# Performance work log

Hardware: AMD Instinct MI355X
Metric: run time of the kernel (lower is better)

## Reference

```python
import jax, jax.numpy as jnp
from jax import lax
import numpy as np

# ---- static config (matches init_kwargs) ----
B, H, W = 8, 32, 32
L = H * W                      # 1024 tokens
D_MODEL = 384
MAMBA_DIM = 192                # d_model * d_mamba_ratio
LOCAL_DIM = 192
D_INNER = 384                  # expand_m * MAMBA_DIM
D_STATE = 16
D_CONV = 4
DT_RANK = 12                   # ceil(MAMBA_DIM / 16)
NDIR = 4                       # h, h_flip, v, v_flip
RED = 48                       # int(D_INNER * 0.125), BiAttn reduce dim
INNER_C = 192                  # LOCAL_DIM * expand_c
K_C = 8                        # local block depthwise kernel size


def setup_inputs() -> dict:
    key = jax.random.key(0)
    ks = jax.random.split(key, 16)
    s = 0.02
    return {
        "x": jax.random.normal(ks[0], (B, L, D_MODEL), jnp.float32),
        "in_proj_w": jax.random.normal(ks[1], (2 * D_INNER, MAMBA_DIM)) * s,
        "A_log": jnp.broadcast_to(jnp.log(jnp.arange(1, D_STATE + 1, dtype=jnp.float32)), (NDIR, D_INNER, D_STATE)) + 0.0,
        "conv_w": jax.random.normal(ks[2], (NDIR, D_INNER, D_CONV)) * 0.2,
        "conv_b": jax.random.normal(ks[3], (NDIR, D_INNER)) * 0.02,
        "xproj_w": jax.random.normal(ks[4], (NDIR, DT_RANK + 2 * D_STATE, D_INNER)) * s,
        "dtproj_w": jax.random.normal(ks[5], (NDIR, D_INNER, DT_RANK)) * (DT_RANK ** -0.5),
        "dtproj_b": jax.random.normal(ks[6], (NDIR, D_INNER)) * 0.5 - 4.0,
        "Dp": jnp.ones((NDIR, D_INNER)),
        "out_proj_w": jax.random.normal(ks[7], (MAMBA_DIM, D_INNER)) * s,
        "attn_ln_g": jnp.ones((D_INNER,)),
        "attn_ln_b": jnp.zeros((D_INNER,)),
        "attn_gr_w": jax.random.normal(ks[8], (RED, D_INNER)) * s,
        "attn_gr_b": jnp.zeros((RED,)),
        "attn_cs_w": jax.random.normal(ks[9], (D_INNER, RED)) * s,
        "attn_cs_b": jnp.zeros((D_INNER,)),
        "pw1_w": jax.random.normal(ks[10], (2 * INNER_C, LOCAL_DIM)) * s,
        "pw1_b": jnp.zeros((2 * INNER_C,)),
        "dw_w": jax.random.normal(ks[11], (INNER_C, K_C)) * 0.2,
        "dw_b": jnp.zeros((INNER_C,)),
        "bn_g": jnp.ones((INNER_C,)),
        "bn_b": jnp.zeros((INNER_C,)),
        "pw2_w": jax.random.normal(ks[12], (LOCAL_DIM, INNER_C)) * s,
        "pw2_b": jnp.zeros((LOCAL_DIM,)),
    }


def _forward(x, in_proj_w, A_log, conv_w, conv_b, xproj_w, dtproj_w, dtproj_b, Dp,
             out_proj_w, attn_ln_g, attn_ln_b, attn_gr_w, attn_gr_b, attn_cs_w, attn_cs_b,
             pw1_w, pw1_b, dw_w, dw_b, bn_g, bn_b, pw2_w, pw2_b):
    mamba_in = x[:, :, :MAMBA_DIM]
    local_in = x[:, :, MAMBA_DIM:]

    # ---------- MultiMamba branch ----------
    xz = jnp.swapaxes(mamba_in @ in_proj_w.T, 1, 2)   # (B, 2*D_INNER, L)

    def to_dir(t, i):
        # reorder channel-last-token axis per scan direction
        if i == 0:
            return t
        if i == 1:
            return jnp.flip(t, -1)
        tv = t.reshape(B, -1, H, W).swapaxes(-1, -2).reshape(B, -1, L)  # column-major scan
        return tv if i == 2 else jnp.flip(tv, -1)

    def from_dir(t, i):
        if i == 0:
            return t
        if i == 1:
            return jnp.flip(t, -1)
        if i == 3:
            t = jnp.flip(t, -1)
        return t.reshape(B, -1, W, H).swapaxes(-1, -2).reshape(B, -1, L)

    def ssm_dir(xzd, i):
        # mamba_inner_fn_no_out_proj: causal dwconv -> silu -> x_proj -> selective scan -> gate
        xp, z = jnp.split(xzd, 2, axis=1)            # (B, D_INNER, L) each
        xpad = jnp.pad(xp, ((0, 0), (0, 0), (D_CONV - 1, 0)))
        u = lax.conv_general_dilated(xpad, conv_w[i][:, None, :], (1,), 'VALID',
                                     dimension_numbers=('NCH', 'OIH', 'NCH'),
                                     feature_group_count=D_INNER)
        u = jax.nn.silu(u + conv_b[i][None, :, None])
        dbl = jnp.einsum('bdl,rd->brl', u, xproj_w[i])
        dt = dbl[:, :DT_RANK]
        Bm = dbl[:, DT_RANK:DT_RANK + D_STATE]
        Cm = dbl[:, DT_RANK + D_STATE:]
        delta = jax.nn.softplus(jnp.einsum('brl,dr->bdl', dt, dtproj_w[i]) + dtproj_b[i][None, :, None])
        A = -jnp.exp(A_log[i])                        # (D_INNER, D_STATE)

        def step(h, inps):
            d_t, B_t, C_t, u_t = inps                 # (B,d),(B,n),(B,n),(B,d)
            h = jnp.exp(d_t[:, :, None] * A) * h + (d_t * u_t)[:, :, None] * B_t[:, None, :]
            return h, jnp.einsum('bdn,bn->bd', h, C_t)

        h0 = jnp.zeros((B, D_INNER, D_STATE), x.dtype)
        _, ys = lax.scan(step, h0, (delta.transpose(2, 0, 1), Bm.transpose(2, 0, 1),
                                    Cm.transpose(2, 0, 1), u.transpose(2, 0, 1)))
        y = ys.transpose(1, 2, 0) + u * Dp[i][:, None]  # (B, D_INNER, L)
        return y * jax.nn.silu(z)

    def biattn(t):                                     # (B, L, D_INNER)
        mu = t.mean(-1, keepdims=True)
        var = ((t - mu) ** 2).mean(-1, keepdims=True)
        tn = (t - mu) / jnp.sqrt(var + 1e-5) * attn_ln_g + attn_ln_b
        g = tn.mean(1, keepdims=True)                  # global pool (B,1,D_INNER)
        g = jax.nn.gelu(g @ attn_gr_w.T + attn_gr_b, approximate=False)
        c = jax.nn.sigmoid(g @ attn_cs_w.T + attn_cs_b)
        return t * c

    acc = jnp.zeros((B, L, D_INNER), x.dtype)
    for i in range(NDIR):                              # fixed small set of directions
        out_i = from_dir(ssm_dir(to_dir(xz, i), i), i)
        acc = acc + biattn(jnp.swapaxes(out_i, 1, 2))
    mamba_out = acc @ out_proj_w.T                     # (B, L, MAMBA_DIM)

    # ---------- Local conv branch ----------
    hch = jnp.einsum('blc,oc->bol', local_in, pw1_w) + pw1_b[None, :, None]
    a, gte = jnp.split(hch, 2, axis=1)
    hch = a * jax.nn.sigmoid(gte)                      # GLU, (B, INNER_C, L)
    pad_l = K_C // 2
    pad_r = K_C // 2 - (K_C + 1) % 2                   # calc_same_padding(8) -> (4, 3)
    hpad = jnp.pad(hch, ((0, 0), (0, 0), (pad_l, pad_r)))
    hch = lax.conv_general_dilated(hpad, dw_w[:, None, :], (1,), 'VALID',
                                   dimension_numbers=('NCH', 'OIH', 'NCH'),
                                   feature_group_count=INNER_C) + dw_b[None, :, None]
    mu = hch.mean((0, 2))                              # BatchNorm1d (training-mode batch stats)
    var = hch.var((0, 2))
    hch = (hch - mu[None, :, None]) / jnp.sqrt(var + 1e-5)[None, :, None] * bn_g[None, :, None] + bn_b[None, :, None]
    hch = hch * jax.nn.sigmoid(hch)                    # Swish
    local_out = jnp.einsum('bcl,oc->blo', hch, pw2_w) + pw2_b

    return jnp.concatenate([mamba_out, local_out], axis=-1)


def reference(x, in_proj_w, A_log, conv_w, conv_b, xproj_w, dtproj_w, dtproj_b, Dp,
              out_proj_w, attn_ln_g, attn_ln_b, attn_gr_w, attn_gr_b, attn_cs_w, attn_cs_b,
              pw1_w, pw1_b, dw_w, dw_b, bn_g, bn_b, pw2_w, pw2_b):
    return _forward(x, in_proj_w, A_log, conv_w, conv_b, xproj_w, dtproj_w, dtproj_b, Dp,
                    out_proj_w, attn_ln_g, attn_ln_b, attn_gr_w, attn_gr_b, attn_cs_w, attn_cs_b,
                    pw1_w, pw1_b, dw_w, dw_b, bn_g, bn_b, pw2_w, pw2_b)
```

## Files before the change

kernel.cpp:

```cpp
#include <hip/hip_runtime.h>
#include <stdint.h>


#define DEV __device__ __forceinline__

typedef __attribute__((ext_vector_type(8))) short short8;
typedef __attribute__((ext_vector_type(4))) short short4v;
typedef __attribute__((ext_vector_type(4))) float f32x4;

DEV float bf(ushort v) { union { uint32_t u; float f; } c; c.u = ((uint32_t)v) << 16; return c.f; }
DEV ushort fbf(float f) {
  union { float f; uint32_t u; } c; c.f = f;
  uint32_t u = c.u;
  return (ushort)((u + 0x7FFFu + ((u >> 16) & 1u)) >> 16);
}

#if __has_builtin(__builtin_amdgcn_exp2f)
DEV float fexp2(float x) { return __builtin_amdgcn_exp2f(x); }
#else
DEV float fexp2(float x) { return __expf(x * 0.6931471805599453f); }
#endif

template<int CTRL>
DEV float rradd(float x) {
  return x + __int_as_float(__builtin_amdgcn_update_dpp(
      0, __float_as_int(x), CTRL, 0xF, 0xF, true));
}

DEV int pmap(int i, int j) {
  if (i == 0) return j;
  if (i == 1) return 1023 - j;
  if (i == 2) return ((j & 31) << 5) | (j >> 5);
  int k = 1023 - j; return ((k & 31) << 5) | (k >> 5);
}

DEV void cvt4(const float* __restrict__ s, ushort* __restrict__ d, int blk, int tid) {
  const int idx = (blk * 256 + tid) * 4;
  float4 v = *(const float4*)(s + idx);
  d[idx] = fbf(v.x); d[idx + 1] = fbf(v.y); d[idx + 2] = fbf(v.z); d[idx + 3] = fbf(v.w);
}

__global__ __launch_bounds__(256) void prep_all(
    const float* __restrict__ x, ushort* __restrict__ xb,
    const float* __restrict__ ipw, ushort* __restrict__ ipwb,
    const float* __restrict__ opw, ushort* __restrict__ opwb,
    const float* __restrict__ pw1w, ushort* __restrict__ pw1wb,
    const float* __restrict__ pw2w, ushort* __restrict__ pw2wb,
    const float* __restrict__ xw, ushort* __restrict__ xwp)
{
  const int bx = blockIdx.x, tid = threadIdx.x;
  if (bx < 3072)      cvt4(x, xb, bx, tid);
  else if (bx < 3216) cvt4(ipw, ipwb, bx - 3072, tid);
  else if (bx < 3288) cvt4(opw, opwb, bx - 3216, tid);
  else if (bx < 3360) cvt4(pw1w, pw1wb, bx - 3288, tid);
  else if (bx < 3396) cvt4(pw2w, pw2wb, bx - 3360, tid);
  else {
    const int row = bx - 3396;
    const int i = row >> 6, nn = row & 63;
    for (int c = tid; c < 384; c += 256)
      xwp[(size_t)row * 384 + c] = (nn < 44) ? fbf(xw[((size_t)i * 44 + nn) * 384 + c]) : (ushort)0;
  }
}

template<bool BF16OUT, bool BIAS>
__global__ __launch_bounds__(256) void gemm_bt(
    const ushort* __restrict__ A, long long sAz, int lda,
    const ushort* __restrict__ Bw, long long sBz,
    const float* __restrict__ bias,
    void* __restrict__ C, long long sCz, int ldc, int coff, int K)
{
  __shared__ ushort As[64][40];
  __shared__ ushort Bs[64][40];
  A += (size_t)blockIdx.z * sAz;
  Bw += (size_t)blockIdx.z * sBz;
  const int tid = threadIdx.x;
  const int m0 = blockIdx.x * 64, n0 = blockIdx.y * 64;
  const int w = tid >> 6, lane = tid & 63, l15 = lane & 15, quad = lane >> 4;
  const int sr = tid >> 2, sc = (tid & 3) * 8;
  f32x4 acc[4] = {};
  for (int k0 = 0; k0 < K; k0 += 32) {
    __syncthreads();
    *(short8*)&As[sr][sc] = *(const short8*)(A + (size_t)(m0 + sr) * lda + k0 + sc);
    *(short8*)&Bs[sr][sc] = *(const short8*)(Bw + (size_t)(n0 + sr) * K + k0 + sc);
    __syncthreads();
    short8 av = *(short8*)&As[w * 16 + l15][quad * 8];
#pragma unroll
    for (int nt = 0; nt < 4; nt++) {
      short8 bv = *(short8*)&Bs[nt * 16 + l15][quad * 8];
      acc[nt] = __builtin_amdgcn_mfma_f32_16x16x32_bf16(av, bv, acc[nt], 0, 0, 0);
    }
  }
  float* cf = (float*)C + (size_t)blockIdx.z * sCz;
  ushort* cb = (ushort*)C + (size_t)blockIdx.z * sCz;
#pragma unroll
  for (int nt = 0; nt < 4; nt++) {
    const int col = n0 + nt * 16 + l15;
    const float bv = BIAS ? bias[col] : 0.f;
#pragma unroll
    for (int r = 0; r < 4; r++) {
      const int row = m0 + w * 16 + quad * 4 + r;
      float v = acc[nt][r] + bv;
      if (BF16OUT) cb[(size_t)row * ldc + coff + col] = fbf(v);
      else         cf[(size_t)row * ldc + coff + col] = v;
    }
  }
}

__global__ __launch_bounds__(256) void gemm_dual(
    const ushort* __restrict__ A0, int lda0, const ushort* __restrict__ B0,
    const float* __restrict__ bias0, void* __restrict__ C0, int ldc0, int coff0, int K0,
    int nt0, int bf0,
    const ushort* __restrict__ A1, int lda1, const ushort* __restrict__ B1,
    const float* __restrict__ bias1, void* __restrict__ C1, int ldc1, int coff1, int K1,
    int bf1)
{
  __shared__ ushort As[64][40];
  __shared__ ushort Bs[64][40];
  const ushort* A; const ushort* Bw; const float* bias; void* C;
  int lda, ldc, coff, K, bf16o, n0;
  if ((int)blockIdx.y < nt0) {
    A = A0; lda = lda0; Bw = B0; bias = bias0; C = C0; ldc = ldc0; coff = coff0; K = K0;
    bf16o = bf0; n0 = blockIdx.y * 64;
  } else {
    A = A1; lda = lda1; Bw = B1; bias = bias1; C = C1; ldc = ldc1; coff = coff1; K = K1;
    bf16o = bf1; n0 = (blockIdx.y - nt0) * 64;
  }
  const int tid = threadIdx.x;
  const int m0 = blockIdx.x * 64;
  const int w = tid >> 6, lane = tid & 63, l15 = lane & 15, quad = lane >> 4;
  const int sr = tid >> 2, sc = (tid & 3) * 8;
  f32x4 acc[4] = {};
  for (int k0 = 0; k0 < K; k0 += 32) {
    __syncthreads();
    *(short8*)&As[sr][sc] = *(const short8*)(A + (size_t)(m0 + sr) * lda + k0 + sc);
    *(short8*)&Bs[sr][sc] = *(const short8*)(Bw + (size_t)(n0 + sr) * K + k0 + sc);
    __syncthreads();
    short8 av = *(short8*)&As[w * 16 + l15][quad * 8];
#pragma unroll
    for (int nt = 0; nt < 4; nt++) {
      short8 bv = *(short8*)&Bs[nt * 16 + l15][quad * 8];
      acc[nt] = __builtin_amdgcn_mfma_f32_16x16x32_bf16(av, bv, acc[nt], 0, 0, 0);
    }
  }
#pragma unroll
  for (int nt = 0; nt < 4; nt++) {
    const int col = n0 + nt * 16 + l15;
    const float bv = bias ? bias[col] : 0.f;
#pragma unroll
    for (int r = 0; r < 4; r++) {
      const int row = m0 + w * 16 + quad * 4 + r;
      float v = acc[nt][r] + bv;
      if (bf16o) ((ushort*)C)[(size_t)row * ldc + coff + col] = fbf(v);
      else       ((float*)C)[(size_t)row * ldc + coff + col] = v;
    }
  }
}

__global__ __launch_bounds__(384) void conv2_kernel(const ushort* __restrict__ xzb,
    const float* __restrict__ cw, const float* __restrict__ cb, ushort* __restrict__ u)
{
  const int d = threadIdx.x;
  const int jt = blockIdx.x;
  const int b = blockIdx.y, i = blockIdx.z;
  __shared__ ushort sx[35][384];
  const int j0 = jt * 32;
#pragma unroll 5
  for (int r = 0; r < 35; r++) {
    const int jj = j0 - 3 + r;
    sx[r][d] = (jj >= 0) ? xzb[(size_t)((b << 10) + pmap(i, jj)) * 768 + d] : (ushort)0;
  }
  __syncthreads();
  const float w0 = cw[((i * 384 + d) << 2) + 0];
  const float w1 = cw[((i * 384 + d) << 2) + 1];
  const float w2 = cw[((i * 384 + d) << 2) + 2];
  const float w3 = cw[((i * 384 + d) << 2) + 3];
  const float cbv = cb[i * 384 + d];
  ushort* ur = u + ((size_t)((i * 8 + b) << 10) + j0) * 384 + d;
#pragma unroll 4
  for (int q = 0; q < 32; q++) {
    float s = bf(sx[q][d]) * w0 + bf(sx[q + 1][d]) * w1 + bf(sx[q + 2][d]) * w2
            + bf(sx[q + 3][d]) * w3 + cbv;
    ur[(size_t)q * 384] = fbf(s / (1.f + __expf(-s)));
  }
}

#define NCH 16
#define CJ 64
__global__ __launch_bounds__(256, 3) void scan7_kernel(
    const ushort* __restrict__ u,
    const float*  __restrict__ dbl,
    const ushort* __restrict__ xzb,
    const float* __restrict__ alog, const float* __restrict__ dtw,
    const float* __restrict__ dtb, const float* __restrict__ Dpw,
    ushort* __restrict__ y)
{
  const int dt0 = blockIdx.x * NCH;
  const int b = blockIdx.y, i = blockIdx.z;
  const int tid = threadIdx.x;
  const int ch = tid >> 4, n = tid & 15;
  const int d = dt0 + ch;
  const int srow = tid >> 2, role = tid & 3;

  __shared__ float sdt[CJ][13];
  __shared__ float su[CJ][20];
  __shared__ float sz[CJ][20];
  __shared__ float sbc[CJ / 2][68];
  __shared__ float sdu[CJ / 2][68];
  __shared__ float sy[CJ][20];
  __shared__ float sDp[NCH];

  float w48[4][12], dtbv4[4];
#pragma unroll
  for (int cc = 0; cc < 4; cc++) {
    const int chp = 4 * role + cc;
#pragma unroll
    for (int r = 0; r < 12; r++) w48[cc][r] = dtw[((size_t)i * 384 + dt0 + chp) * 12 + r];
    dtbv4[cc] = dtb[i * 384 + dt0 + chp];
  }
  const float L2E = 1.4426950408889634f;
  const float Al = -__expf(alog[((size_t)i * 384 + d) * 16 + n]) * L2E;
  if (tid < NCH) sDp[tid] = Dpw[i * 384 + dt0 + tid];

  const size_t rb = (size_t)(i * 8 + b) << 10;
  const ushort* ub = u + rb * 384 + dt0;
  const float* dblb = dbl + rb * 64;
  const ushort* zb = xzb + ((size_t)b << 10) * 768 + 384 + dt0;
  ushort* yb = y + rb * 384 + dt0;
  const float* sdup = &sdu[0][4 * ch];
  const float* sbcp = &sbc[0][4 * n];

  float h = 0.f;

  for (int c = 0; c < 16; c++) {
    const int j0 = c * CJ;
    __syncthreads();
    {
      const float* src = dblb + (size_t)(j0 + srow) * 64 + role * 12;
      f32x4 r0 = *(const f32x4*)(src);
      f32x4 r1 = *(const f32x4*)(src + 4);
      f32x4 r2 = *(const f32x4*)(src + 8);
      if (role == 0) {
#pragma unroll
        for (int k = 0; k < 4; k++) {
          sdt[srow][k] = r0[k]; sdt[srow][4 + k] = r1[k]; sdt[srow][8 + k] = r2[k];
        }
      } else {
        float vals[12];
#pragma unroll
        for (int k = 0; k < 4; k++) { vals[k] = r0[k]; vals[4 + k] = r1[k]; vals[8 + k] = r2[k]; }
#pragma unroll
        for (int k = 0; k < 12; k++) {
          const int f = role * 12 + k;
          if (f < 44) {
            const int isC = (f >= 28) ? 1 : 0;
            const int nn = isC ? (f - 28) : (f - 12);
            sbc[srow >> 1][4 * nn + 2 * (srow & 1) + isC] = vals[k];
          }
        }
      }
    }
    {
      const short4v u4 = *(const short4v*)(ub + (size_t)(j0 + srow) * 384 + 4 * role);
      const int lo = pmap(i, j0 + srow);
      const short4v z4 = *(const short4v*)(zb + (size_t)lo * 768 + 4 * role);
      f32x4 uf, zf;
#pragma unroll
      for (int k = 0; k < 4; k++) { uf[k] = bf((ushort)u4[k]); zf[k] = bf((ushort)z4[k]); }
      *(f32x4*)&su[srow][4 * role] = uf;
      *(f32x4*)&sz[srow][4 * role] = zf;
    }
    __syncthreads();
    {
      float dtr[12];
#pragma unroll
      for (int k = 0; k < 12; k++) dtr[k] = sdt[srow][k];
#pragma unroll
      for (int cc = 0; cc < 4; cc++) {
        const int chp = 4 * role + cc;
        float s = dtbv4[cc];
#pragma unroll
        for (int r = 0; r < 12; r++) s += dtr[r] * w48[cc][r];
        const float dl = fmaxf(s, 0.f) + __logf(1.f + __expf(-fabsf(s)));
        float2 pr; pr.x = dl; pr.y = dl * su[srow][chp];
        *(float2*)&sdu[srow >> 1][4 * chp + 2 * (srow & 1)] = pr;
      }
    }
    __syncthreads();
#pragma unroll
    for (int q = 0; q < 4; q++) {
      float pq = 0.f;
#pragma unroll
      for (int s2 = 0; s2 < 8; s2++) {
        const f32x4 duP = *(const f32x4*)(sdup + q * 544 + s2 * 68);
        const f32x4 bcP = *(const f32x4*)(sbcp + q * 544 + s2 * 68);
        {
          const float e = fexp2(duP[0] * Al);
          h = e * h + duP[1] * bcP[0];
          float p = h * bcP[1];
          p = rradd<0x128>(p); p = rradd<0x124>(p); p = rradd<0x122>(p); p = rradd<0x121>(p);
          pq = (n == 2 * s2) ? p : pq;
        }
        {
          const float e = fexp2(duP[2] * Al);
          h = e * h + duP[3] * bcP[2];
          float p = h * bcP[3];
          p = rradd<0x128>(p); p = rradd<0x124>(p); p = rradd<0x122>(p); p = rradd<0x121>(p);
          pq = (n == 2 * s2 + 1) ? p : pq;
        }
      }
      sy[(q << 4) | n][ch] = pq;
    }
    __syncthreads();
    {
      const int lo = pmap(i, j0 + srow);
      const f32x4 y4 = *(const f32x4*)&sy[srow][role * 4];
      const f32x4 u4 = *(const f32x4*)&su[srow][role * 4];
      const f32x4 z4 = *(const f32x4*)&sz[srow][role * 4];
      short4v o;
#pragma unroll
      for (int t = 0; t < 4; t++) {
        const float z = z4[t];
        const float val = (y4[t] + u4[t] * sDp[role * 4 + t]) * (z / (1.f + __expf(-z)));
        o[t] = (short)fbf(val);
      }
      *(short4v*)(yb + (size_t)lo * 384 + role * 4) = o;
    }
  }
}

__global__ __launch_bounds__(256) void lngm_kernel(const ushort* __restrict__ y,
                                                   float* __restrict__ G16)
{
  const int slab = blockIdx.x, b = blockIdx.y, i = blockIdx.z;
  const int tid = threadIdx.x;
  const int w = tid >> 6, lane = tid & 63;
  __shared__ float smu[64], srs[64];
  const size_t base = (size_t)i * 8192 + b * 1024 + slab * 64;
  for (int rr = 0; rr < 16; rr++) {
    const int r = w * 16 + rr;
    const ushort* yr = y + (base + r) * 384;
    float s = 0.f, ss = 0.f;
#pragma unroll
    for (int t = 0; t < 6; t++) { float v = bf(yr[lane + (t << 6)]); s += v; ss += v * v; }
#pragma unroll
    for (int off = 1; off < 64; off <<= 1) { s += __shfl_xor(s, off, 64); ss += __shfl_xor(ss, off, 64); }
    if (lane == 0) {
      float m = s * (1.f / 384.f);
      float va = ss * (1.f / 384.f) - m * m;
      smu[r] = m;
      srs[r] = rsqrtf(va + 1e-5f);
    }
  }
  __syncthreads();
  for (int col = tid; col < 384; col += 256) {
    float s = 0.f;
    for (int r = 0; r < 64; r++)
      s += (bf(y[(base + r) * 384 + col]) - smu[r]) * srs[r];
    G16[((size_t)(i * 8 + b) * 16 + slab) * 384 + col] = s;
  }
}

__global__ __launch_bounds__(64) void gate_kernel(const float* __restrict__ G16,
    const float* __restrict__ lng, const float* __restrict__ lnb,
    const float* __restrict__ grw, const float* __restrict__ grb,
    const float* __restrict__ csw, const float* __restrict__ csb, float* __restrict__ cbuf)
{
  const int b = blockIdx.x, i = blockIdx.y;
  const int ib = i * 8 + b;
  const int lane = threadIdx.x;
  __shared__ float sG[384];
  __shared__ float g48[48];
  for (int dd = lane; dd < 384; dd += 64) {
    const float* g = G16 + (size_t)ib * 16 * 384 + dd;
    float s = 0.f;
#pragma unroll
    for (int k = 0; k < 16; k++) s += g[k * 384];
    sG[dd] = s * (1.f / 1024.f) * lng[dd] + lnb[dd];
  }
  __syncthreads();
  if (lane < 48) {
    float s = grb[lane];
    for (int dd = 0; dd < 384; dd++) s += sG[dd] * grw[lane * 384 + dd];
    g48[lane] = 0.5f * s * (1.f + erff(s * 0.70710678118f));
  }
  __syncthreads();
  for (int dd = lane; dd < 384; dd += 64) {
    float s = csb[dd];
#pragma unroll
    for (int r = 0; r < 48; r++) s += g48[r] * csw[dd * 48 + r];
    cbuf[(size_t)ib * 384 + dd] = 1.f / (1.f + __expf(-s));
  }
}

__global__ void accgate_kernel(const ushort* __restrict__ y, const float* __restrict__ cbuf,
                               ushort* __restrict__ accb)
{
  const int d = threadIdx.x;
  const int row = blockIdx.x;
  const int b = row >> 10;
  float s = 0.f;
#pragma unroll
  for (int i = 0; i < 4; i++)
    s += bf(y[((size_t)i * 8192 + row) * 384 + d]) * cbuf[(size_t)(i * 8 + b) * 384 + d];
  accb[(size_t)row * 384 + d] = fbf(s);
}

__global__ __launch_bounds__(192) void gludwbn_kernel(const ushort* __restrict__ hchb,
    const float* __restrict__ dww, const float* __restrict__ dwb,
    float* __restrict__ h2, float* __restrict__ bnsum)
{
  const int c = threadIdx.x;
  const int lt = blockIdx.x, b = blockIdx.y;
  float wk[8];
#pragma unroll
  for (int k = 0; k < 8; k++) wk[k] = dww[(c << 3) + k];
  const float bias = dwb[c];
  float sacc = 0.f, ssacc = 0.f;
  for (int q = 0; q < 32; q++) {
    const int l = lt * 32 + q;
    float s = bias;
#pragma unroll
    for (int k = 0; k < 8; k++) {
      const int ls = l + k - 4;
      if (ls >= 0 && ls < 1024) {
        const size_t rr = (size_t)((b << 10) + ls) * 384;
        const float a = bf(hchb[rr + c]);
        const float g = bf(hchb[rr + 192 + c]);
        s += (a / (1.f + __expf(-g))) * wk[k];
      }
    }
    h2[(size_t)((b << 10) + l) * 192 + c] = s;
    sacc += s; ssacc += s * s;
  }
  atomicAdd(&bnsum[c], sacc);
  atomicAdd(&bnsum[192 + c], ssacc);
}

__global__ void bnact_kernel(const float* __restrict__ h2, const float* __restrict__ bnsum,
                             const float* __restrict__ bng, const float* __restrict__ bnb,
                             ushort* __restrict__ sbuf)
{
  const int c = threadIdx.x;
  const int row = blockIdx.x;
  float m = bnsum[c] * (1.f / 8192.f);
  float va = bnsum[192 + c] * (1.f / 8192.f) - m * m;
  float x = (h2[(size_t)row * 192 + c] - m) * rsqrtf(va + 1e-5f) * bng[c] + bnb[c];
  sbuf[(size_t)row * 192 + c] = fbf(x / (1.f + __expf(-x)));
}

extern "C" void kernel_launch(void* const* d_in, const int* in_sizes, int n_in,
                              void* d_out, int out_size, void* d_ws, size_t ws_size,
                              hipStream_t stream) {
  const float* x    = (const float*)d_in[0];
  const float* ipw  = (const float*)d_in[1];
  const float* alog = (const float*)d_in[2];
  const float* cw   = (const float*)d_in[3];
  const float* cbv  = (const float*)d_in[4];
  const float* xw   = (const float*)d_in[5];
  const float* dtw  = (const float*)d_in[6];
  const float* dtb  = (const float*)d_in[7];
  const float* Dpw  = (const float*)d_in[8];
  const float* opw  = (const float*)d_in[9];
  const float* lng  = (const float*)d_in[10];
  const float* lnb  = (const float*)d_in[11];
  const float* grw  = (const float*)d_in[12];
  const float* grb  = (const float*)d_in[13];
  const float* csw  = (const float*)d_in[14];
  const float* csb  = (const float*)d_in[15];
  const float* pw1w = (const float*)d_in[16];
  const float* pw1b = (const float*)d_in[17];
  const float* dww  = (const float*)d_in[18];
  const float* dwb  = (const float*)d_in[19];
  const float* bng  = (const float*)d_in[20];
  const float* bnb  = (const float*)d_in[21];
  const float* pw2w = (const float*)d_in[22];
  const float* pw2b = (const float*)d_in[23];
  float* out = (float*)d_out;

  char* ws = (char*)d_ws;
  ushort* xb    = (ushort*)(ws + 0);
  ushort* xzb   = (ushort*)(ws + 6291456);
  ushort* u     = (ushort*)(ws + 18874368);
  float*  dbl   = (float*)(ws + 44040192);
  ushort* y     = (ushort*)(ws + 52428800);
  ushort* accb  = (ushort*)(ws + 77594624);
  float*  G16   = (float*)(ws + 83886080);
  float*  cbuf  = (float*)(ws + 84672512);
  ushort* xwp   = (ushort*)(ws + 84721664);
  ushort* ipwb  = (ushort*)(ws + 84918272);
  ushort* opwb  = (ushort*)(ws + 85213184);
  ushort* pw1wb = (ushort*)(ws + 85360640);
  ushort* pw2wb = (ushort*)(ws + 85508096);
  float*  bnsum = (float*)(ws + 85581824);
  ushort* hchb = (ushort*)(ws + 18874368);
  float*  h2   = (float*)(ws + 34603008);
  ushort* sbuf = (ushort*)(ws + 40894464);

  prep_all<<<dim3(3652), 256, 0, stream>>>(x, xb, ipw, ipwb, opw, opwb,
                                           pw1w, pw1wb, pw2w, pw2wb, xw, xwp);
  gemm_bt<true, false><<<dim3(128, 12, 1), 256, 0, stream>>>(
      xb, 0, 384, ipwb, 0, nullptr, xzb, 0, 768, 0, 192);
  conv2_kernel<<<dim3(32, 8, 4), 384, 0, stream>>>(xzb, cw, cbv, u);
  gemm_bt<false, false><<<dim3(128, 1, 4), 256, 0, stream>>>(
      u, 8192LL * 384, 384, xwp, 64LL * 384, nullptr, dbl, 8192LL * 64, 64, 0, 384);
  scan7_kernel<<<dim3(24, 8, 4), 256, 0, stream>>>(u, dbl, xzb, alog, dtw, dtb, Dpw, y);
  lngm_kernel<<<dim3(16, 8, 4), 256, 0, stream>>>(y, G16);
  gate_kernel<<<dim3(8, 4), 64, 0, stream>>>(G16, lng, lnb, grw, grb, csw, csb, cbuf);
  accgate_kernel<<<dim3(8192), 384, 0, stream>>>(y, cbuf, accb);
  gemm_dual<<<dim3(128, 9), 256, 0, stream>>>(
      accb, 384, opwb, nullptr, out, 384, 0, 384, 3, 0,
      xb + 192, 384, pw1wb, pw1b, hchb, 384, 0, 192, 1);
  (void)hipMemsetAsync(bnsum, 0, 384 * sizeof(float), stream);
  gludwbn_kernel<<<dim3(32, 8), 192, 0, stream>>>(hchb, dww, dwb, h2, bnsum);
  bnact_kernel<<<dim3(8192), 192, 0, stream>>>(h2, bnsum, bng, bnb, sbuf);
  gemm_bt<false, true><<<dim3(128, 3, 1), 256, 0, stream>>>(
      sbuf, 0, 192, pw2wb, 0, pw2b, out, 0, 384, 192, 192);
}
```

Baseline: 369.3 us.

## Cut scan reduction shuffles, vectorize LN/accgate loads, stage GLU in shared memory

In the selective scan, the per-step 16-lane reduction drops from four row-rotate adds to two. Partial sums are accumulated into four lanes-per-group slots with mask FMAs and finished by two DPP swaps once per q-chunk. The LayerNorm statistics loop and the accumulate-gate kernel now use vectorized bf16 loads, with accgate handling four rows per block. The GLU+depthwise conv kernel computes each GLU value once into a shared tile, instead of recomputing the sigmoid eight times per output. These changes aim to remove redundant cross-lane ops, scalar memory transactions and repeated exp/loads, at the cost of more shared memory and extra FMAs per step.

```diff
diff --git a/kernel.cpp b/kernel.cpp
--- a/kernel.cpp
+++ b/kernel.cpp
@@ -186,7 +186,7 @@
 
 #define NCH 16
 #define CJ 64
-__global__ __launch_bounds__(256, 3) void scan7_kernel(
+__global__ __launch_bounds__(256, 3) void scan8_kernel(
     const ushort* __restrict__ u,
     const float*  __restrict__ dbl,
     const ushort* __restrict__ xzb,
@@ -220,6 +220,9 @@
   const float L2E = 1.4426950408889634f;
   const float Al = -__expf(alog[((size_t)i * 384 + d) * 16 + n]) * L2E;
   if (tid < NCH) sDp[tid] = Dpw[i * 384 + dt0 + tid];
+
+  const float selm[4] = { (n >> 2) == 0 ? 1.f : 0.f, (n >> 2) == 1 ? 1.f : 0.f,
+                          (n >> 2) == 2 ? 1.f : 0.f, (n >> 2) == 3 ? 1.f : 0.f };
 
   const size_t rb = (size_t)(i * 8 + b) << 10;
   const ushort* ub = u + rb * 384 + dt0;
@@ -288,27 +291,32 @@
     __syncthreads();
 #pragma unroll
     for (int q = 0; q < 4; q++) {
-      float pq = 0.f;
+      f32x4 pq = {0.f, 0.f, 0.f, 0.f};
 #pragma unroll
       for (int s2 = 0; s2 < 8; s2++) {
-        const f32x4 duP = *(const f32x4*)(sdup + q * 544 + s2 * 68);
-        const f32x4 bcP = *(const f32x4*)(sbcp + q * 544 + s2 * 68);
+        const f32x4 duP = *(const f32x4*)(sdup + (q * 8 + s2) * 68);
+        const f32x4 bcP = *(const f32x4*)(sbcp + (q * 8 + s2) * 68);
         {
           const float e = fexp2(duP[0] * Al);
           h = e * h + duP[1] * bcP[0];
           float p = h * bcP[1];
-          p = rradd<0x128>(p); p = rradd<0x124>(p); p = rradd<0x122>(p); p = rradd<0x121>(p);
-          pq = (n == 2 * s2) ? p : pq;
+          p = rradd<0x124>(p); p = rradd<0x128>(p);
+          pq[s2 >> 1] = fmaf(selm[(2 * s2) & 3], p, pq[s2 >> 1]);
         }
         {
           const float e = fexp2(duP[2] * Al);
           h = e * h + duP[3] * bcP[2];
           float p = h * bcP[3];
-          p = rradd<0x128>(p); p = rradd<0x124>(p); p = rradd<0x122>(p); p = rradd<0x121>(p);
-          pq = (n == 2 * s2 + 1) ? p : pq;
+          p = rradd<0x124>(p); p = rradd<0x128>(p);
+          pq[s2 >> 1] = fmaf(selm[(2 * s2 + 1) & 3], p, pq[s2 >> 1]);
         }
       }
-      sy[(q << 4) | n][ch] = pq;
+#pragma unroll
+      for (int j = 0; j < 4; j++) {
+        float t2 = rradd<0xB1>(pq[j]);
+        t2 = rradd<0x4E>(t2);
+        if ((n & 3) == 0) sy[(q << 4) | (j << 2) | (n >> 2)][ch] = t2;
+      }
     }
     __syncthreads();
     {
@@ -340,8 +348,12 @@
     const int r = w * 16 + rr;
     const ushort* yr = y + (base + r) * 384;
     float s = 0.f, ss = 0.f;
-#pragma unroll
-    for (int t = 0; t < 6; t++) { float v = bf(yr[lane + (t << 6)]); s += v; ss += v * v; }
+    const short4v v4 = *(const short4v*)(yr + 4 * lane);
+    const uint32_t v2 = *(const uint32_t*)(yr + 256 + 2 * lane);
+#pragma unroll
+    for (int t = 0; t < 4; t++) { float v = bf((ushort)v4[t]); s += v; ss += v * v; }
+    { float v = bf((ushort)(v2 & 0xffffu)); s += v; ss += v * v; }
+    { float v = bf((ushort)(v2 >> 16));     s += v; ss += v * v; }
 #pragma unroll
     for (int off = 1; off < 64; off <<= 1) { s += __shfl_xor(s, off, 64); ss += __shfl_xor(ss, off, 64); }
     if (lane == 0) {
@@ -392,17 +404,25 @@
   }
 }
 
-__global__ void accgate_kernel(const ushort* __restrict__ y, const float* __restrict__ cbuf,
-                               ushort* __restrict__ accb)
-{
-  const int d = threadIdx.x;
-  const int row = blockIdx.x;
+__global__ __launch_bounds__(384) void accgate_kernel(const ushort* __restrict__ y,
+    const float* __restrict__ cbuf, ushort* __restrict__ accb)
+{
+  const int t = threadIdx.x;
+  const int row = blockIdx.x * 4 + (t / 96);
+  const int cg = (t % 96) * 4;
   const int b = row >> 10;
-  float s = 0.f;
-#pragma unroll
-  for (int i = 0; i < 4; i++)
-    s += bf(y[((size_t)i * 8192 + row) * 384 + d]) * cbuf[(size_t)(i * 8 + b) * 384 + d];
-  accb[(size_t)row * 384 + d] = fbf(s);
+  f32x4 s = {};
+#pragma unroll
+  for (int i = 0; i < 4; i++) {
+    const short4v v = *(const short4v*)(y + ((size_t)i * 8192 + row) * 384 + cg);
+    const f32x4 cv = *(const f32x4*)(cbuf + (size_t)(i * 8 + b) * 384 + cg);
+#pragma unroll
+    for (int k = 0; k < 4; k++) s[k] += bf((ushort)v[k]) * cv[k];
+  }
+  short4v o;
+#pragma unroll
+  for (int k = 0; k < 4; k++) o[k] = (short)fbf(s[k]);
+  *(short4v*)(accb + (size_t)row * 384 + cg) = o;
 }
 
 __global__ __launch_bounds__(192) void gludwbn_kernel(const ushort* __restrict__ hchb,
@@ -411,25 +431,31 @@
 {
   const int c = threadIdx.x;
   const int lt = blockIdx.x, b = blockIdx.y;
+  __shared__ float sv[39][192];
+  const int l0 = lt * 32;
+#pragma unroll 4
+  for (int r = 0; r < 39; r++) {
+    const int ls = l0 + r - 4;
+    float v = 0.f;
+    if (ls >= 0 && ls < 1024) {
+      const size_t rr = (size_t)((b << 10) + ls) * 384;
+      const float a = bf(hchb[rr + c]);
+      const float g = bf(hchb[rr + 192 + c]);
+      v = a / (1.f + __expf(-g));
+    }
+    sv[r][c] = v;
+  }
+  __syncthreads();
   float wk[8];
 #pragma unroll
   for (int k = 0; k < 8; k++) wk[k] = dww[(c << 3) + k];
   const float bias = dwb[c];
   float sacc = 0.f, ssacc = 0.f;
   for (int q = 0; q < 32; q++) {
-    const int l = lt * 32 + q;
     float s = bias;
 #pragma unroll
-    for (int k = 0; k < 8; k++) {
-      const int ls = l + k - 4;
-      if (ls >= 0 && ls < 1024) {
-        const size_t rr = (size_t)((b << 10) + ls) * 384;
-        const float a = bf(hchb[rr + c]);
-        const float g = bf(hchb[rr + 192 + c]);
-        s += (a / (1.f + __expf(-g))) * wk[k];
-      }
-    }
-    h2[(size_t)((b << 10) + l) * 192 + c] = s;
+    for (int k = 0; k < 8; k++) s += sv[q + k][c] * wk[k];
+    h2[(size_t)((b << 10) + l0 + q) * 192 + c] = s;
     sacc += s; ssacc += s * s;
   }
   atomicAdd(&bnsum[c], sacc);
@@ -503,10 +529,10 @@
   conv2_kernel<<<dim3(32, 8, 4), 384, 0, stream>>>(xzb, cw, cbv, u);
   gemm_bt<false, false><<<dim3(128, 1, 4), 256, 0, stream>>>(
       u, 8192LL * 384, 384, xwp, 64LL * 384, nullptr, dbl, 8192LL * 64, 64, 0, 384);
-  scan7_kernel<<<dim3(24, 8, 4), 256, 0, stream>>>(u, dbl, xzb, alog, dtw, dtb, Dpw, y);
+  scan8_kernel<<<dim3(24, 8, 4), 256, 0, stream>>>(u, dbl, xzb, alog, dtw, dtb, Dpw, y);
   lngm_kernel<<<dim3(16, 8, 4), 256, 0, stream>>>(y, G16);
   gate_kernel<<<dim3(8, 4), 64, 0, stream>>>(G16, lng, lnb, grw, grb, csw, csb, cbuf);
-  accgate_kernel<<<dim3(8192), 384, 0, stream>>>(y, cbuf, accb);
+  accgate_kernel<<<dim3(2048), 384, 0, stream>>>(y, cbuf, accb);
   gemm_dual<<<dim3(128, 9), 256, 0, stream>>>(
       accb, 384, opwb, nullptr, out, 384, 0, 384, 3, 0,
       xb + 192, 384, pw1wb, pw1b, hchb, 384, 0, 192, 1);
```

After: 333.9 us. 9.6% less time.
